# Kernel tuning notes

Hardware: AMD Instinct MI355X
Metric: run time of the kernel (lower is better)

Reference implementation:

```python
import jax, jax.numpy as jnp
import numpy as np

EPS = 1e-6
NUM_HEADS = 12

def _ln(x, s, b):
    mu = jnp.mean(x, -1, keepdims=True)
    var = jnp.mean((x - mu) ** 2, -1, keepdims=True)
    return (x - mu) * jax.lax.rsqrt(var + EPS) * s + b

def _forward(x, patch_w, patch_b, cls_token, pos_embed, ln1_s, ln1_b, qkv_w, qkv_b,
             proj_w, proj_b, ln2_s, ln2_b, fc1_w, fc1_b, fc2_w, fc2_b, lnf_s, lnf_b):
    B, C, Hi, Wi = x.shape
    E = patch_w.shape[0]
    p = patch_w.shape[-1]
    gh, gw = Hi // p, Wi // p  # 14, 14
    hd = E // NUM_HEADS
    scale = hd ** -0.5
    # patch embedding: strided conv == block reshape + contraction
    xp = x.reshape(B, C, gh, p, gw, p)
    tok = jnp.einsum('bchpwq,ecpq->bhwe', xp, patch_w).reshape(B, gh * gw, E) + patch_b
    x = jnp.concatenate([jnp.broadcast_to(cls_token, (B, 1, E)), tok], axis=1) + pos_embed

    def block(xc, params):
        l1s, l1b, qw, qb, pw, pb, l2s, l2b, f1w, f1b, f2w, f2b = params
        y = _ln(xc, l1s, l1b)
        N = y.shape[1]
        qkv = (y @ qw + qb).reshape(B, N, 3, NUM_HEADS, hd)
        q, k, v = jnp.moveaxis(qkv, 2, 0)            # each [B,N,H,d]
        q = jnp.swapaxes(q, 1, 2)                     # [B,H,N,d]
        k = jnp.swapaxes(k, 1, 2)
        v = jnp.swapaxes(v, 1, 2)
        attn = jax.nn.softmax(jnp.einsum('bhnd,bhmd->bhnm', q, k) * scale, axis=-1)
        # extra head-averaged attention stats (as in original Attention.forward)
        cls_attn = jnp.mean(attn[:, :, 0, :], axis=1)          # [B,N]
        patch_attn = jnp.mean(attn[:, :, :, 1:], axis=1)       # [B,N,N-1]
        cls_patch = jnp.mean(patch_attn * cls_attn[:, :, None], axis=1).reshape(B, 1, 14, 14)
        attn_back = jnp.mean(attn, axis=1, keepdims=True)      # [B,1,N,N]
        o = jnp.einsum('bhnm,bhmd->bnhd', attn, v).reshape(B, N, E)
        xc = xc + (o @ pw + pb)
        h = _ln(xc, l2s, l2b)
        h = jax.nn.gelu(h @ f1w + f1b, approximate=False) @ f2w + f2b
        xc = xc + h
        return xc, (attn_back, cls_patch)

    x, (attn_backs, cls_patches) = jax.lax.scan(
        block, x, (ln1_s, ln1_b, qkv_w, qkv_b, proj_w, proj_b, ln2_s, ln2_b,
                   fc1_w, fc1_b, fc2_w, fc2_b))
    x = _ln(x, lnf_s, lnf_b)
    # pre_logits = Identity, head = None in this repo; return cls features
    # plus last block's attention stats (the custom-kernel-relevant outputs)
    return x[:, 0], attn_backs[-1], cls_patches[-1]

def setup_inputs() -> dict:
    key = jax.random.key(0)
    ks = jax.random.split(key, 8)
    B, E, Dff, P, depth, N = 32, 768, 3072, 16, 12, 197
    def nrm(k, shape, s=0.02):
        return jax.random.normal(k, shape, jnp.float32) * s
    return dict(
        x=jax.random.normal(ks[0], (B, 3, 224, 224), jnp.float32),
        patch_w=nrm(ks[1], (E, 3, P, P)), patch_b=jnp.zeros((E,), jnp.float32),
        cls_token=nrm(ks[2], (1, 1, E)), pos_embed=nrm(ks[3], (1, N, E)),
        ln1_s=jnp.ones((depth, E), jnp.float32), ln1_b=jnp.zeros((depth, E), jnp.float32),
        qkv_w=nrm(ks[4], (depth, E, 3 * E)), qkv_b=jnp.zeros((depth, 3 * E), jnp.float32),
        proj_w=nrm(ks[5], (depth, E, E)), proj_b=jnp.zeros((depth, E), jnp.float32),
        ln2_s=jnp.ones((depth, E), jnp.float32), ln2_b=jnp.zeros((depth, E), jnp.float32),
        fc1_w=nrm(ks[6], (depth, E, Dff)), fc1_b=jnp.zeros((depth, Dff), jnp.float32),
        fc2_w=nrm(ks[7], (depth, Dff, E)), fc2_b=jnp.zeros((depth, E), jnp.float32),
        lnf_s=jnp.ones((E,), jnp.float32), lnf_b=jnp.zeros((E,), jnp.float32))

def reference(x, patch_w, patch_b, cls_token, pos_embed, ln1_s, ln1_b, qkv_w, qkv_b,
              proj_w, proj_b, ln2_s, ln2_b, fc1_w, fc1_b, fc2_w, fc2_b, lnf_s, lnf_b):
    return _forward(x, patch_w, patch_b, cls_token, pos_embed, ln1_s, ln1_b, qkv_w, qkv_b,
                    proj_w, proj_b, ln2_s, ln2_b, fc1_w, fc1_b, fc2_w, fc2_b, lnf_s, lnf_b)
```

## Files before the change

### kernel.cpp

```cpp
#include <hip/hip_runtime.h>
#include <math.h>

typedef unsigned short u16;
typedef __bf16 bf16x8 __attribute__((ext_vector_type(8)));
typedef float f32x4 __attribute__((ext_vector_type(4)));

#define NPAD 224
#define NTOK 197
#define NH_ 12
#define E_ 768
#define B_ 32
#define MROWS (B_*NPAD)

__device__ __forceinline__ u16 f2bf(float f) {
    union { float f; unsigned u; } x; x.f = f;
    unsigned r = x.u + 0x7fffu + ((x.u >> 16) & 1u);
    return (u16)(r >> 16);
}
__device__ __forceinline__ float bf2f(u16 s) {
    union { unsigned u; float f; } x; x.u = ((unsigned)s) << 16;
    return x.f;
}

template<int EPI>
__global__ __launch_bounds__(256, 2) void gemm_bf16(
    const u16* __restrict__ A, const u16* __restrict__ W,
    const float* __restrict__ bias, void* __restrict__ Cout,
    const float* __restrict__ aux, int M, int N, int K)
{
    __shared__ u16 lds_a[128*32];
    __shared__ u16 lds_b[128*32];
    const int tid = threadIdx.x;
    const int lane = tid & 63;
    const int wm = (tid >> 7);
    const int wn = (tid >> 6) & 1;
    const int m0 = blockIdx.x * 128, n0 = blockIdx.y * 128;
    const int l15 = lane & 15, g8 = (lane >> 4) << 3;
    f32x4 acc[4][4] = {};
    for (int k0 = 0; k0 < K; k0 += 32) {
        #pragma unroll
        for (int it = 0; it < 2; ++it) {
            int flat = it*256 + tid;
            int row = flat >> 2, kb = (flat & 3) << 3;
            *(uint4*)&lds_a[row*32 + kb] = *(const uint4*)&A[(size_t)(m0+row)*K + k0 + kb];
            *(uint4*)&lds_b[row*32 + kb] = *(const uint4*)&W[(size_t)(n0+row)*K + k0 + kb];
        }
        __syncthreads();
        bf16x8 af[4], bfr[4];
        #pragma unroll
        for (int i = 0; i < 4; ++i)
            af[i] = *(const bf16x8*)&lds_a[(wm*64 + i*16 + l15)*32 + g8];
        #pragma unroll
        for (int j = 0; j < 4; ++j)
            bfr[j] = *(const bf16x8*)&lds_b[(wn*64 + j*16 + l15)*32 + g8];
        #pragma unroll
        for (int i = 0; i < 4; ++i)
            #pragma unroll
            for (int j = 0; j < 4; ++j)
                acc[i][j] = __builtin_amdgcn_mfma_f32_16x16x32_bf16(af[i], bfr[j], acc[i][j], 0, 0, 0);
        __syncthreads();
    }
    const int r0 = (lane >> 4) << 2;
    #pragma unroll
    for (int i = 0; i < 4; ++i) {
        #pragma unroll
        for (int j = 0; j < 4; ++j) {
            #pragma unroll
            for (int r = 0; r < 4; ++r) {
                int row = m0 + wm*64 + i*16 + r0 + r;
                int col = n0 + wn*64 + j*16 + l15;
                float v = acc[i][j][r] + bias[col];
                if constexpr (EPI == 1) {
                    ((u16*)Cout)[(size_t)row*N + col] = f2bf(v);
                } else if constexpr (EPI == 2) {
                    ((float*)Cout)[(size_t)row*N + col] += v;
                } else if constexpr (EPI == 3) {
                    float gv = 0.5f * v * (1.0f + erff(v * 0.70710678118f));
                    ((u16*)Cout)[(size_t)row*N + col] = f2bf(gv);
                } else if constexpr (EPI == 4) {
                    int b = row / 196, t = 1 + row % 196;
                    ((float*)Cout)[((size_t)(b*NPAD + t))*E_ + col] = v + aux[(size_t)t*E_ + col];
                }
            }
        }
    }
}

__global__ __launch_bounds__(256) void transpose_w(
    const float* __restrict__ in, u16* __restrict__ out, int R, int C)
{
    __shared__ u16 t[32][33];
    int r0 = blockIdx.x*32, c0 = blockIdx.y*32;
    int tr = threadIdx.x >> 5, tc = threadIdx.x & 31;
    #pragma unroll
    for (int i = 0; i < 4; ++i)
        t[tr + 8*i][tc] = f2bf(in[(size_t)(r0 + tr + 8*i)*C + c0 + tc]);
    __syncthreads();
    #pragma unroll
    for (int i = 0; i < 4; ++i)
        out[(size_t)(c0 + tr + 8*i)*R + r0 + tc] = t[tc][tr + 8*i];
}

__global__ __launch_bounds__(256) void cvt_w(const float* __restrict__ in, u16* __restrict__ out, int n4)
{
    int i = blockIdx.x*256 + threadIdx.x;
    if (i < n4) {
        float4 v = ((const float4*)in)[i];
        unsigned lo = (unsigned)f2bf(v.x) | ((unsigned)f2bf(v.y) << 16);
        unsigned hi = (unsigned)f2bf(v.z) | ((unsigned)f2bf(v.w) << 16);
        ((uint2*)out)[i] = make_uint2(lo, hi);
    }
}

__global__ __launch_bounds__(192) void gather_patches(const float* __restrict__ x, u16* __restrict__ Ap)
{
    int m = blockIdx.x; int b = m / 196, loc = m % 196;
    int gh = loc / 14, gw = loc % 14;
    int kk = threadIdx.x * 4;
    int c = kk >> 8, rem = kk & 255, p = rem >> 4, q = rem & 15;
    const float* src = &x[(size_t)((b*3 + c)*224 + gh*16 + p)*224 + gw*16 + q];
    float4 v = *(const float4*)src;
    unsigned lo = (unsigned)f2bf(v.x) | ((unsigned)f2bf(v.y) << 16);
    unsigned hi = (unsigned)f2bf(v.z) | ((unsigned)f2bf(v.w) << 16);
    *(uint2*)&Ap[(size_t)m*768 + kk] = make_uint2(lo, hi);
}

__global__ __launch_bounds__(256) void init_x(const float* __restrict__ cls,
                                              const float* __restrict__ pos, float* __restrict__ X)
{
    int b = blockIdx.y, xi = blockIdx.x, tid = threadIdx.x;
    if (xi == 0) {
        #pragma unroll
        for (int i = 0; i < 3; ++i) {
            int e = tid + 256*i;
            X[(size_t)(b*NPAD)*E_ + e] = cls[e] + pos[e];
        }
    } else {
        int t = 196 + xi;
        #pragma unroll
        for (int i = 0; i < 3; ++i)
            X[((size_t)(b*NPAD + t))*E_ + tid + 256*i] = 0.0f;
    }
}

template<int FINAL>
__global__ __launch_bounds__(256) void ln_rows(
    const float* __restrict__ X, const float* __restrict__ s,
    const float* __restrict__ bb, void* __restrict__ Y)
{
    int row = FINAL ? blockIdx.x * NPAD : blockIdx.x;
    int t = row % NPAD;
    int tid = threadIdx.x, lane = tid & 63, wave = tid >> 6;
    __shared__ float red[8];
    if (!FINAL && t >= NTOK) {
        u16* yp = (u16*)Y + (size_t)row*E_;
        #pragma unroll
        for (int i = 0; i < 3; ++i) yp[tid + 256*i] = 0;
        return;
    }
    const float* xr = X + (size_t)row*E_;
    float v0 = xr[tid], v1 = xr[tid+256], v2 = xr[tid+512];
    float s1 = v0+v1+v2;
    #pragma unroll
    for (int off = 32; off; off >>= 1) s1 += __shfl_xor(s1, off);
    if (lane == 0) red[wave] = s1;
    __syncthreads();
    float mu = (red[0]+red[1]+red[2]+red[3]) * (1.0f/768.0f);
    float d0 = v0-mu, d1 = v1-mu, d2 = v2-mu;
    float s2 = d0*d0 + d1*d1 + d2*d2;
    #pragma unroll
    for (int off = 32; off; off >>= 1) s2 += __shfl_xor(s2, off);
    if (lane == 0) red[4+wave] = s2;
    __syncthreads();
    float rs = rsqrtf((red[4]+red[5]+red[6]+red[7]) * (1.0f/768.0f) + 1e-6f);
    if (FINAL) {
        float* yp = (float*)Y + (size_t)blockIdx.x*E_;
        yp[tid]     = d0*rs*s[tid]     + bb[tid];
        yp[tid+256] = d1*rs*s[tid+256] + bb[tid+256];
        yp[tid+512] = d2*rs*s[tid+512] + bb[tid+512];
    } else {
        u16* yp = (u16*)Y + (size_t)row*E_;
        yp[tid]     = f2bf(d0*rs*s[tid]     + bb[tid]);
        yp[tid+256] = f2bf(d1*rs*s[tid+256] + bb[tid+256]);
        yp[tid+512] = f2bf(d2*rs*s[tid+512] + bb[tid+512]);
    }
}

__global__ __launch_bounds__(256) void attn_sm(
    const u16* __restrict__ QKV, u16* __restrict__ P)
{
    __shared__ u16 kt[208*64];
    int bh = blockIdx.y, b = bh / NH_, h = bh % NH_;
    int tid = threadIdx.x, lane = tid & 63, wave = tid >> 6;
    const size_t base = (size_t)b * NPAD * 2304;
    for (int it = 0; it < 7; ++it) {
        int flat = it*256 + tid;
        if (flat < 1664) {
            int tok = flat >> 3, ch = (flat & 7) << 3;
            *(uint4*)&kt[tok*64 + ch] =
                *(const uint4*)&QKV[base + (size_t)tok*2304 + 768 + h*64 + ch];
        }
    }
    __syncthreads();
    int i0 = blockIdx.x*64 + wave*16;
    if (i0 >= NPAD) return;
    int l15 = lane & 15, g8 = (lane >> 4) << 3;
    const u16* qp = &QKV[base + (size_t)(i0 + l15)*2304 + h*64];
    bf16x8 q0 = *(const bf16x8*)&qp[g8];
    bf16x8 q1 = *(const bf16x8*)&qp[32 + g8];
    f32x4 c[13];
    #pragma unroll
    for (int jt = 0; jt < 13; ++jt) {
        f32x4 z = {};
        bf16x8 k0 = *(const bf16x8*)&kt[(jt*16 + l15)*64 + g8];
        bf16x8 k1 = *(const bf16x8*)&kt[(jt*16 + l15)*64 + 32 + g8];
        z = __builtin_amdgcn_mfma_f32_16x16x32_bf16(q0, k0, z, 0, 0, 0);
        z = __builtin_amdgcn_mfma_f32_16x16x32_bf16(q1, k1, z, 0, 0, 0);
        c[jt] = z;
    }
    #pragma unroll
    for (int r = 0; r < 4; ++r) {
        float mx = -1e30f;
        #pragma unroll
        for (int jt = 0; jt < 13; ++jt) {
            float v = c[jt][r] * 0.125f;
            if (jt*16 + l15 >= NTOK) v = -1e30f;
            c[jt][r] = v;
            mx = fmaxf(mx, v);
        }
        #pragma unroll
        for (int msk = 1; msk <= 8; msk <<= 1) mx = fmaxf(mx, __shfl_xor(mx, msk));
        float sm = 0.0f;
        #pragma unroll
        for (int jt = 0; jt < 13; ++jt) {
            float e = __expf(c[jt][r] - mx);
            c[jt][r] = e; sm += e;
        }
        #pragma unroll
        for (int msk = 1; msk <= 8; msk <<= 1) sm += __shfl_xor(sm, msk);
        float inv = 1.0f / sm;
        int prow = i0 + (lane >> 4)*4 + r;
        size_t pb = ((size_t)bh*NPAD + prow)*NPAD;
        #pragma unroll
        for (int jt = 0; jt < 13; ++jt)
            P[pb + jt*16 + l15] = f2bf(c[jt][r] * inv);
        P[pb + 208 + l15] = 0;
    }
}

__global__ __launch_bounds__(256) void attn_pv(
    const u16* __restrict__ QKV, const u16* __restrict__ P, u16* __restrict__ O)
{
    __shared__ u16 vt[64*232];
    int bh = blockIdx.y, b = bh / NH_, h = bh % NH_;
    int tid = threadIdx.x, lane = tid & 63, wave = tid >> 6;
    const size_t vbase = (size_t)b * NPAD * 2304 + 1536 + h*64;
    int d = tid & 63, grp = tid >> 6;
    for (int it = 0; it < 14; ++it) {
        int tok0 = (it*4 + grp)*4;
        u16 t0 = QKV[vbase + (size_t)(tok0+0)*2304 + d];
        u16 t1 = QKV[vbase + (size_t)(tok0+1)*2304 + d];
        u16 t2 = QKV[vbase + (size_t)(tok0+2)*2304 + d];
        u16 t3 = QKV[vbase + (size_t)(tok0+3)*2304 + d];
        unsigned lo = (unsigned)t0 | ((unsigned)t1 << 16);
        unsigned hi = (unsigned)t2 | ((unsigned)t3 << 16);
        *(uint2*)&vt[d*232 + tok0] = make_uint2(lo, hi);
    }
    __syncthreads();
    int i0 = blockIdx.x*32 + (wave >> 1)*16;
    int d0 = (wave & 1)*32;
    int l15 = lane & 15, g8 = (lane >> 4) << 3;
    f32x4 acc0 = {}, acc1 = {};
    size_t pr = ((size_t)bh*NPAD + i0 + l15)*NPAD;
    #pragma unroll
    for (int kt = 0; kt < 7; ++kt) {
        bf16x8 pa = *(const bf16x8*)&P[pr + kt*32 + g8];
        bf16x8 v0 = *(const bf16x8*)&vt[(d0 + l15)*232 + kt*32 + g8];
        bf16x8 v1 = *(const bf16x8*)&vt[(d0 + 16 + l15)*232 + kt*32 + g8];
        acc0 = __builtin_amdgcn_mfma_f32_16x16x32_bf16(pa, v0, acc0, 0, 0, 0);
        acc1 = __builtin_amdgcn_mfma_f32_16x16x32_bf16(pa, v1, acc1, 0, 0, 0);
    }
    int r0 = (lane >> 4) << 2;
    #pragma unroll
    for (int r = 0; r < 4; ++r) {
        int row = i0 + r0 + r;
        size_t ob = (size_t)(b*NPAD + row)*E_ + h*64;
        O[ob + d0 + l15]      = f2bf(acc0[r]);
        O[ob + d0 + 16 + l15] = f2bf(acc1[r]);
    }
}

__global__ __launch_bounds__(256) void attn_mean(const u16* __restrict__ P, float* __restrict__ out)
{
    int i = blockIdx.x, b = blockIdx.y;
    int j = threadIdx.x;
    if (j >= NTOK) return;
    float s = 0.0f;
    #pragma unroll
    for (int h = 0; h < NH_; ++h)
        s += bf2f(P[((size_t)(b*NH_ + h)*NPAD + i)*NPAD + j]);
    out[24576 + ((size_t)b*NTOK + i)*NTOK + j] = s * (1.0f/12.0f);
}

__global__ __launch_bounds__(256) void cls_patch_k(const float* __restrict__ ab, float* __restrict__ out)
{
    int b = blockIdx.x, tid = threadIdx.x;
    __shared__ float cls[NTOK];
    if (tid < NTOK) cls[tid] = ab[((size_t)b*NTOK + 0)*NTOK + tid];
    __syncthreads();
    if (tid < 196) {
        float s = 0.0f;
        for (int n = 0; n < NTOK; ++n)
            s += ab[((size_t)b*NTOK + n)*NTOK + tid + 1] * cls[n];
        out[1266464 + b*196 + tid] = s * (1.0f/197.0f);
    }
}

extern "C" void kernel_launch(void* const* d_in, const int* in_sizes, int n_in,
                              void* d_out, int out_size, void* d_ws, size_t ws_size,
                              hipStream_t stream) {
    const float* x        = (const float*)d_in[0];
    const float* patch_w  = (const float*)d_in[1];
    const float* patch_b  = (const float*)d_in[2];
    const float* cls_tok  = (const float*)d_in[3];
    const float* pos_emb  = (const float*)d_in[4];
    const float* ln1_s    = (const float*)d_in[5];
    const float* ln1_b    = (const float*)d_in[6];
    const float* qkv_w    = (const float*)d_in[7];
    const float* qkv_b    = (const float*)d_in[8];
    const float* proj_w   = (const float*)d_in[9];
    const float* proj_b   = (const float*)d_in[10];
    const float* ln2_s    = (const float*)d_in[11];
    const float* ln2_b    = (const float*)d_in[12];
    const float* fc1_w    = (const float*)d_in[13];
    const float* fc1_b    = (const float*)d_in[14];
    const float* fc2_w    = (const float*)d_in[15];
    const float* fc2_b    = (const float*)d_in[16];
    const float* lnf_s    = (const float*)d_in[17];
    const float* lnf_b    = (const float*)d_in[18];

    char* w = (char*)d_ws;
    float* X  = (float*)(w);
    u16*   Y  = (u16*)  (w + 22020096);
    u16*  QKV = (u16*)  (w + 33030144);
    u16*   P  = (u16*)  (w + 66060288);
    u16*   H  = (u16*)  (w + 104595456);
    u16*   Wt = (u16*)  (w + 148635648);
    u16*   O  = H;
    u16*   Ap = H;
    float* out = (float*)d_out;

    gather_patches<<<6272, 192, 0, stream>>>(x, Ap);
    cvt_w<<<576, 256, 0, stream>>>(patch_w, Wt, 768*768/4);
    init_x<<<dim3(28, 32), 256, 0, stream>>>(cls_tok, pos_emb, X);
    gemm_bf16<4><<<dim3(49, 6), 256, 0, stream>>>(Ap, Wt, patch_b, X, pos_emb, 6272, 768, 768);

    for (int l = 0; l < 12; ++l) {
        ln_rows<0><<<MROWS, 256, 0, stream>>>(X, ln1_s + (size_t)l*768, ln1_b + (size_t)l*768, Y);
        transpose_w<<<dim3(24, 72), 256, 0, stream>>>(qkv_w + (size_t)l*768*2304, Wt, 768, 2304);
        gemm_bf16<1><<<dim3(56, 18), 256, 0, stream>>>(Y, Wt, qkv_b + (size_t)l*2304, QKV, nullptr, MROWS, 2304, 768);
        attn_sm<<<dim3(4, 384), 256, 0, stream>>>(QKV, P);
        attn_pv<<<dim3(7, 384), 256, 0, stream>>>(QKV, P, O);
        transpose_w<<<dim3(24, 24), 256, 0, stream>>>(proj_w + (size_t)l*768*768, Wt, 768, 768);
        gemm_bf16<2><<<dim3(56, 6), 256, 0, stream>>>(O, Wt, proj_b + (size_t)l*768, X, nullptr, MROWS, 768, 768);
        ln_rows<0><<<MROWS, 256, 0, stream>>>(X, ln2_s + (size_t)l*768, ln2_b + (size_t)l*768, Y);
        transpose_w<<<dim3(24, 96), 256, 0, stream>>>(fc1_w + (size_t)l*768*3072, Wt, 768, 3072);
        gemm_bf16<3><<<dim3(56, 24), 256, 0, stream>>>(Y, Wt, fc1_b + (size_t)l*3072, H, nullptr, MROWS, 3072, 768);
        transpose_w<<<dim3(96, 24), 256, 0, stream>>>(fc2_w + (size_t)l*3072*768, Wt, 3072, 768);
        gemm_bf16<2><<<dim3(56, 6), 256, 0, stream>>>(H, Wt, fc2_b + (size_t)l*768, X, nullptr, MROWS, 768, 3072);
    }

    attn_mean<<<dim3(197, 32), 256, 0, stream>>>(P, out);
    cls_patch_k<<<32, 256, 0, stream>>>(out + 24576, out);
    ln_rows<1><<<32, 256, 0, stream>>>(X, lnf_s, lnf_b, out);
}
```

Measured before the change: 3.851 ms.

## Use direct global-to-LDS loads in GEMM, batch weight transposes, wave-per-row layernorm

The GEMM tile loads now use global_load_lds to copy A and W tiles straight into shared memory, skipping the register round trip. The four per-layer weight transposes are merged into one launch that writes into separate Wt regions. LayerNorm now uses one wave per row with float4 loads and shuffle-only reductions, so block-level syncs go away. Together these cut launch count and load overhead, but the merged transpose needs more workspace and the LDS-direct path relies on the 16-byte global_load_lds variant being available on this target.

```diff
diff --git a/kernel.cpp b/kernel.cpp
--- a/kernel.cpp
+++ b/kernel.cpp
@@ -21,6 +21,10 @@
     union { unsigned u; float f; } x; x.u = ((unsigned)s) << 16;
     return x.f;
 }
+__device__ __forceinline__ void gload16(const void* g, void* l) {
+    __builtin_amdgcn_global_load_lds((const __attribute__((address_space(1))) void*)g,
+                                     (__attribute__((address_space(3))) void*)l, 16, 0, 0);
+}
 
 template<int EPI>
 __global__ __launch_bounds__(256, 2) void gemm_bf16(
@@ -32,19 +36,23 @@
     __shared__ u16 lds_b[128*32];
     const int tid = threadIdx.x;
     const int lane = tid & 63;
-    const int wm = (tid >> 7);
-    const int wn = (tid >> 6) & 1;
+    const int wid = tid >> 6;
+    const int wm = wid >> 1, wn = wid & 1;
     const int m0 = blockIdx.x * 128, n0 = blockIdx.y * 128;
     const int l15 = lane & 15, g8 = (lane >> 4) << 3;
+    const int srow = lane >> 2;
+    const int scol = (lane & 3) << 3;
+    const u16* gA = &A[(size_t)(m0 + wid*32 + srow)*K + scol];
+    const u16* gB = &W[(size_t)(n0 + wid*32 + srow)*K + scol];
+    u16* dA = &lds_a[wid*32*32];
+    u16* dB = &lds_b[wid*32*32];
     f32x4 acc[4][4] = {};
     for (int k0 = 0; k0 < K; k0 += 32) {
-        #pragma unroll
-        for (int it = 0; it < 2; ++it) {
-            int flat = it*256 + tid;
-            int row = flat >> 2, kb = (flat & 3) << 3;
-            *(uint4*)&lds_a[row*32 + kb] = *(const uint4*)&A[(size_t)(m0+row)*K + k0 + kb];
-            *(uint4*)&lds_b[row*32 + kb] = *(const uint4*)&W[(size_t)(n0+row)*K + k0 + kb];
-        }
+        gload16(gA,        dA);
+        gload16(gA + 16*K, dA + 512);
+        gload16(gB,        dB);
+        gload16(gB + 16*K, dB + 512);
+        gA += 32; gB += 32;
         __syncthreads();
         bf16x8 af[4], bfr[4];
         #pragma unroll
@@ -86,11 +94,20 @@
     }
 }
 
-__global__ __launch_bounds__(256) void transpose_w(
-    const float* __restrict__ in, u16* __restrict__ out, int R, int C)
+__global__ __launch_bounds__(256) void trans_all(
+    const float* __restrict__ qkv_w, const float* __restrict__ proj_w,
+    const float* __restrict__ fc1_w, const float* __restrict__ fc2_w,
+    u16* __restrict__ Wt)
 {
     __shared__ u16 t[32][33];
-    int r0 = blockIdx.x*32, c0 = blockIdx.y*32;
+    int id = blockIdx.x;
+    const float* in; u16* out; int R, C, lid;
+    if (id < 1728)      { in = qkv_w;  out = Wt;           R = 768;  C = 2304; lid = id; }
+    else if (id < 2304) { in = proj_w; out = Wt + 1769472; R = 768;  C = 768;  lid = id - 1728; }
+    else if (id < 4608) { in = fc1_w;  out = Wt + 2359296; R = 768;  C = 3072; lid = id - 2304; }
+    else                { in = fc2_w;  out = Wt + 4718592; R = 3072; C = 768;  lid = id - 4608; }
+    int nR = R >> 5;
+    int r0 = (lid % nR) << 5, c0 = (lid / nR) << 5;
     int tr = threadIdx.x >> 5, tc = threadIdx.x & 31;
     #pragma unroll
     for (int i = 0; i < 4; ++i)
@@ -148,41 +165,50 @@
     const float* __restrict__ X, const float* __restrict__ s,
     const float* __restrict__ bb, void* __restrict__ Y)
 {
-    int row = FINAL ? blockIdx.x * NPAD : blockIdx.x;
-    int t = row % NPAD;
-    int tid = threadIdx.x, lane = tid & 63, wave = tid >> 6;
-    __shared__ float red[8];
-    if (!FINAL && t >= NTOK) {
-        u16* yp = (u16*)Y + (size_t)row*E_;
-        #pragma unroll
-        for (int i = 0; i < 3; ++i) yp[tid + 256*i] = 0;
+    const int lane = threadIdx.x & 63, wv = threadIdx.x >> 6;
+    const int r = blockIdx.x*4 + wv;
+    const int row = FINAL ? r*NPAD : r;
+    if (!FINAL && (row % NPAD) >= NTOK) {
+        uint2* yp = (uint2*)((u16*)Y + (size_t)row*E_);
+        uint2 z = make_uint2(0u, 0u);
+        yp[lane] = z; yp[lane+64] = z; yp[lane+128] = z;
         return;
     }
-    const float* xr = X + (size_t)row*E_;
-    float v0 = xr[tid], v1 = xr[tid+256], v2 = xr[tid+512];
-    float s1 = v0+v1+v2;
+    const float4* xr = (const float4*)(X + (size_t)row*E_);
+    float4 a0 = xr[lane], a1 = xr[lane+64], a2 = xr[lane+128];
+    float s1 = a0.x+a0.y+a0.z+a0.w + a1.x+a1.y+a1.z+a1.w + a2.x+a2.y+a2.z+a2.w;
     #pragma unroll
     for (int off = 32; off; off >>= 1) s1 += __shfl_xor(s1, off);
-    if (lane == 0) red[wave] = s1;
-    __syncthreads();
-    float mu = (red[0]+red[1]+red[2]+red[3]) * (1.0f/768.0f);
-    float d0 = v0-mu, d1 = v1-mu, d2 = v2-mu;
-    float s2 = d0*d0 + d1*d1 + d2*d2;
+    float mu = s1 * (1.0f/768.0f);
+    float d0x=a0.x-mu, d0y=a0.y-mu, d0z=a0.z-mu, d0w=a0.w-mu;
+    float d1x=a1.x-mu, d1y=a1.y-mu, d1z=a1.z-mu, d1w=a1.w-mu;
+    float d2x=a2.x-mu, d2y=a2.y-mu, d2z=a2.z-mu, d2w=a2.w-mu;
+    float s2 = d0x*d0x+d0y*d0y+d0z*d0z+d0w*d0w
+             + d1x*d1x+d1y*d1y+d1z*d1z+d1w*d1w
+             + d2x*d2x+d2y*d2y+d2z*d2z+d2w*d2w;
     #pragma unroll
     for (int off = 32; off; off >>= 1) s2 += __shfl_xor(s2, off);
-    if (lane == 0) red[4+wave] = s2;
-    __syncthreads();
-    float rs = rsqrtf((red[4]+red[5]+red[6]+red[7]) * (1.0f/768.0f) + 1e-6f);
+    float rs = rsqrtf(s2 * (1.0f/768.0f) + 1e-6f);
+    const float4* sp = (const float4*)s;
+    const float4* bp = (const float4*)bb;
+    float4 s0v = sp[lane], s1v = sp[lane+64], s2v = sp[lane+128];
+    float4 b0v = bp[lane], b1v = bp[lane+64], b2v = bp[lane+128];
+    float o0x=d0x*rs*s0v.x+b0v.x, o0y=d0y*rs*s0v.y+b0v.y, o0z=d0z*rs*s0v.z+b0v.z, o0w=d0w*rs*s0v.w+b0v.w;
+    float o1x=d1x*rs*s1v.x+b1v.x, o1y=d1y*rs*s1v.y+b1v.y, o1z=d1z*rs*s1v.z+b1v.z, o1w=d1w*rs*s1v.w+b1v.w;
+    float o2x=d2x*rs*s2v.x+b2v.x, o2y=d2y*rs*s2v.y+b2v.y, o2z=d2z*rs*s2v.z+b2v.z, o2w=d2w*rs*s2v.w+b2v.w;
     if (FINAL) {
-        float* yp = (float*)Y + (size_t)blockIdx.x*E_;
-        yp[tid]     = d0*rs*s[tid]     + bb[tid];
-        yp[tid+256] = d1*rs*s[tid+256] + bb[tid+256];
-        yp[tid+512] = d2*rs*s[tid+512] + bb[tid+512];
+        float4* yp = (float4*)((float*)Y + (size_t)r*E_);
+        yp[lane]     = make_float4(o0x,o0y,o0z,o0w);
+        yp[lane+64]  = make_float4(o1x,o1y,o1z,o1w);
+        yp[lane+128] = make_float4(o2x,o2y,o2z,o2w);
     } else {
-        u16* yp = (u16*)Y + (size_t)row*E_;
-        yp[tid]     = f2bf(d0*rs*s[tid]     + bb[tid]);
-        yp[tid+256] = f2bf(d1*rs*s[tid+256] + bb[tid+256]);
-        yp[tid+512] = f2bf(d2*rs*s[tid+512] + bb[tid+512]);
+        uint2* yp = (uint2*)((u16*)Y + (size_t)row*E_);
+        yp[lane]     = make_uint2((unsigned)f2bf(o0x) | ((unsigned)f2bf(o0y)<<16),
+                                  (unsigned)f2bf(o0z) | ((unsigned)f2bf(o0w)<<16));
+        yp[lane+64]  = make_uint2((unsigned)f2bf(o1x) | ((unsigned)f2bf(o1y)<<16),
+                                  (unsigned)f2bf(o1z) | ((unsigned)f2bf(o1w)<<16));
+        yp[lane+128] = make_uint2((unsigned)f2bf(o2x) | ((unsigned)f2bf(o2y)<<16),
+                                  (unsigned)f2bf(o2z) | ((unsigned)f2bf(o2w)<<16));
     }
 }
 
@@ -356,21 +382,19 @@
     gemm_bf16<4><<<dim3(49, 6), 256, 0, stream>>>(Ap, Wt, patch_b, X, pos_emb, 6272, 768, 768);
 
     for (int l = 0; l < 12; ++l) {
-        ln_rows<0><<<MROWS, 256, 0, stream>>>(X, ln1_s + (size_t)l*768, ln1_b + (size_t)l*768, Y);
-        transpose_w<<<dim3(24, 72), 256, 0, stream>>>(qkv_w + (size_t)l*768*2304, Wt, 768, 2304);
+        trans_all<<<6912, 256, 0, stream>>>(qkv_w + (size_t)l*1769472, proj_w + (size_t)l*589824,
+                                            fc1_w + (size_t)l*2359296, fc2_w + (size_t)l*2359296, Wt);
+        ln_rows<0><<<1792, 256, 0, stream>>>(X, ln1_s + (size_t)l*768, ln1_b + (size_t)l*768, Y);
         gemm_bf16<1><<<dim3(56, 18), 256, 0, stream>>>(Y, Wt, qkv_b + (size_t)l*2304, QKV, nullptr, MROWS, 2304, 768);
         attn_sm<<<dim3(4, 384), 256, 0, stream>>>(QKV, P);
         attn_pv<<<dim3(7, 384), 256, 0, stream>>>(QKV, P, O);
-        transpose_w<<<dim3(24, 24), 256, 0, stream>>>(proj_w + (size_t)l*768*768, Wt, 768, 768);
-        gemm_bf16<2><<<dim3(56, 6), 256, 0, stream>>>(O, Wt, proj_b + (size_t)l*768, X, nullptr, MROWS, 768, 768);
-        ln_rows<0><<<MROWS, 256, 0, stream>>>(X, ln2_s + (size_t)l*768, ln2_b + (size_t)l*768, Y);
-        transpose_w<<<dim3(24, 96), 256, 0, stream>>>(fc1_w + (size_t)l*768*3072, Wt, 768, 3072);
-        gemm_bf16<3><<<dim3(56, 24), 256, 0, stream>>>(Y, Wt, fc1_b + (size_t)l*3072, H, nullptr, MROWS, 3072, 768);
-        transpose_w<<<dim3(96, 24), 256, 0, stream>>>(fc2_w + (size_t)l*3072*768, Wt, 3072, 768);
-        gemm_bf16<2><<<dim3(56, 6), 256, 0, stream>>>(H, Wt, fc2_b + (size_t)l*768, X, nullptr, MROWS, 768, 3072);
+        gemm_bf16<2><<<dim3(56, 6), 256, 0, stream>>>(O, Wt + 1769472, proj_b + (size_t)l*768, X, nullptr, MROWS, 768, 768);
+        ln_rows<0><<<1792, 256, 0, stream>>>(X, ln2_s + (size_t)l*768, ln2_b + (size_t)l*768, Y);
+        gemm_bf16<3><<<dim3(56, 24), 256, 0, stream>>>(Y, Wt + 2359296, fc1_b + (size_t)l*3072, H, nullptr, MROWS, 3072, 768);
+        gemm_bf16<2><<<dim3(56, 6), 256, 0, stream>>>(H, Wt + 4718592, fc2_b + (size_t)l*768, X, nullptr, MROWS, 768, 3072);
     }
 
     attn_mean<<<dim3(197, 32), 256, 0, stream>>>(P, out);
     cls_patch_k<<<32, 256, 0, stream>>>(out + 24576, out);
-    ln_rows<1><<<32, 256, 0, stream>>>(X, lnf_s, lnf_b, out);
-}
+    ln_rows<1><<<8, 256, 0, stream>>>(X, lnf_s, lnf_b, out);
+}
```

After: 3.606 ms. -6.4%, faster.
